# Performance work log

Measured on AMD Instinct MI355X. Metric: run time of the kernel, lower is better.

The kernel has to match this reference:

```python
import jax, jax.numpy as jnp
import numpy as np

EPS = 1e-5   # BatchNorm eps (eval mode, running_mean=0, running_var=1 as at init)
NEG = 0.2    # LeakyReLU negative slope


def _conv(W, x):
    # 1x1 conv == channel matmul. W: [out_c, in_c], x: [B, in_c, ...]
    return jnp.einsum('oc,bc...->bo...', W, x)


def _bn(x, g, b):
    # eval-mode BN with running_mean=0, running_var=1
    sh = (1, -1) + (1,) * (x.ndim - 2)
    return x * (g.reshape(sh) / np.float32(np.sqrt(1.0 + EPS))) + b.reshape(sh)


def _lrelu(x):
    return jax.nn.leaky_relu(x, NEG)


def _knn_idx(pos, k):
    # pos: [B, 3, N] -> idx [B, N, k] of k nearest points (incl. self)
    sq = jnp.sum(pos * pos, axis=1)                      # [B, N]
    inner = jnp.einsum('bcn,bcm->bnm', pos, pos)         # [B, N, N]
    dist = sq[:, :, None] + sq[:, None, :] - 2.0 * inner
    _, idx = jax.lax.top_k(-dist, k)
    return idx


def _gather(points, idx):
    # points [B, N, C], idx [B, N, K] -> [B, N, K, C]
    return jax.vmap(lambda p, i: p[i])(points, idx)


def setup_inputs() -> dict:
    key = jax.random.key(0)
    B, N, K = 2, 8192, 16
    d_points, d_model = 64, 64
    ks = jax.random.split(key, 24)
    w = lambda k_, o, i: (jax.random.normal(k_, (o, i), jnp.float32) * 0.05)
    gm = lambda k_, c: (1.0 + 0.1 * jax.random.normal(k_, (c,), jnp.float32))
    bt = lambda k_, c: (0.1 * jax.random.normal(k_, (c,), jnp.float32))
    return {
        'feats': jax.random.normal(ks[0], (B, d_points, N), jnp.float32),
        'pos': jax.random.uniform(ks[1], (B, 3, N), jnp.float32),
        'k': K,
        'W1': w(ks[2], d_model, d_points), 'g1': gm(ks[3], d_model), 'b1': bt(ks[4], d_model),
        'Wq': w(ks[5], d_model, d_model), 'Wk': w(ks[6], d_model, d_model), 'Wv': w(ks[7], d_model, d_model),
        'Wd1': w(ks[8], d_model, 3), 'gd1': gm(ks[9], d_model), 'bd1': bt(ks[10], d_model),
        'Wd2': w(ks[11], d_model, d_model), 'gd2': gm(ks[12], d_model), 'bd2': bt(ks[13], d_model),
        'Wg1': w(ks[14], d_model, d_model), 'gg1': gm(ks[15], d_model), 'bg1': bt(ks[16], d_model),
        'Wg2': w(ks[17], d_model, d_model), 'gg2': gm(ks[18], d_model), 'bg2': bt(ks[19], d_model),
        'W2': w(ks[20], d_points, d_model), 'g2': gm(ks[21], d_points), 'b2': bt(ks[22], d_points),
    }


def reference(feats, pos, k, W1, g1, b1, Wq, Wk, Wv,
              Wd1, gd1, bd1, Wd2, gd2, bd2,
              Wg1, gg1, bg1, Wg2, gg2, bg2, W2, g2, b2):
    B, _, N = feats.shape
    knn_idx = _knn_idx(pos, k)                            # [B, N, K]
    pos_nc = jnp.transpose(pos, (0, 2, 1))                # [B, N, 3]
    knn_pos = _gather(pos_nc, knn_idx)                    # [B, N, K, 3]

    x = _lrelu(_bn(_conv(W1, feats), g1, b1))             # [B, d, N]
    q = _conv(Wq, x)                                      # [B, d, N]
    k_feat = _gather(jnp.transpose(_conv(Wk, x), (0, 2, 1)), knn_idx)
    k_t = jnp.transpose(k_feat, (0, 3, 2, 1))             # [B, d, K, N]
    v_feat = _gather(jnp.transpose(_conv(Wv, x), (0, 2, 1)), knn_idx)
    v_t = jnp.transpose(v_feat, (0, 3, 2, 1))             # [B, d, K, N]

    rel = pos_nc[:, :, None, :] - knn_pos                 # [B, N, K, 3]
    rel_t = jnp.transpose(rel, (0, 3, 2, 1))              # [B, 3, K, N]
    pe = _lrelu(_bn(_conv(Wd1, rel_t), gd1, bd1))
    pos_enc = _lrelu(_bn(_conv(Wd2, pe), gd2, bd2))       # [B, d, K, N]

    a = q[:, :, None, :] - k_t + pos_enc                  # [B, d, K, N]
    a = _lrelu(_bn(_conv(Wg1, a), gg1, bg1))
    a = _lrelu(_bn(_conv(Wg2, a), gg2, bg2))
    # torch: attn / sqrt(k.size(-1)) where k has shape [B, d, K, N] -> sqrt(N)
    attn = jax.nn.softmax(a / jnp.sqrt(jnp.float32(N)), axis=-2)

    res = jnp.einsum('bmnf,bmnf->bmf', attn, v_t + pos_enc)  # [B, d, N]
    out = _lrelu(_bn(_conv(W2, res), g2, b2)) + feats
    return out
```

## Files before the change

kernel.cpp:

```cpp
#include <hip/hip_runtime.h>
#include <hip/hip_bf16.h>
#include <math.h>

namespace {

constexpr int B = 2;
constexpr int N = 8192;
constexpr int D = 64;
constexpr int GRID = 10;
constexpr int GC = GRID * GRID * GRID;
constexpr float H = 0.1f;
constexpr float NEGS = 0.2f;
constexpr float BN_INV = 0.9999950000374997f;
constexpr float RSQN = 0.011048543456039806f;

typedef __attribute__((ext_vector_type(8))) short bf16x8;
typedef __attribute__((ext_vector_type(16))) float f32x16;

union Frag { int4 i4; unsigned u[4]; bf16x8 h; };

__device__ __forceinline__ float lrelu(float v) { return fmaxf(v, NEGS * v); }

__device__ __forceinline__ unsigned pk2(float a, float b) {
  __hip_bfloat162 h2 = __float22bfloat162_rn(make_float2(a, b));
  unsigned r;
  __builtin_memcpy(&r, &h2, 4);
  return r;
}
__device__ __forceinline__ float blo(unsigned u) { return __uint_as_float(u << 16); }
__device__ __forceinline__ float bhi(unsigned u) { return __uint_as_float(u & 0xFFFF0000u); }

__device__ __forceinline__ f32x16 MF(int4 a, const Frag& b, f32x16 c) {
  Frag af; af.i4 = a;
  return __builtin_amdgcn_mfma_f32_32x32x16_bf16(af.h, b.h, c, 0, 0, 0);
}

template <int CTRL>
__device__ __forceinline__ float dpp_add(float v) {
  int t = __builtin_amdgcn_update_dpp(0, __float_as_int(v), CTRL, 0xF, 0xF, false);
  return v + __int_as_float(t);
}
__device__ __forceinline__ float rsum16(float v) {
  v = dpp_add<0x128>(v);
  v = dpp_add<0x124>(v);
  v = dpp_add<0x122>(v);
  v = dpp_add<0x121>(v);
  return v;
}
template <int CTRL>
__device__ __forceinline__ unsigned long long dpp_min_u64(unsigned long long k) {
  int lo = __builtin_amdgcn_update_dpp(0, (int)(unsigned)k, CTRL, 0xF, 0xF, false);
  int hi = __builtin_amdgcn_update_dpp(0, (int)(unsigned)(k >> 32), CTRL, 0xF, 0xF, false);
  unsigned long long o = ((unsigned long long)(unsigned)hi << 32) | (unsigned)lo;
  return o < k ? o : k;
}
__device__ __forceinline__ unsigned long long rmin16_u64(unsigned long long k) {
  k = dpp_min_u64<0x128>(k);
  k = dpp_min_u64<0x124>(k);
  k = dpp_min_u64<0x122>(k);
  k = dpp_min_u64<0x121>(k);
  return k;
}

__device__ __forceinline__ int cellco(float v) {
  int c = (int)(v * 10.0f);
  return min(max(c, 0), GRID - 1);
}

__device__ __forceinline__ void buildB(const f32x16& x0, const f32x16& x1, int h, Frag Bf[4]) {
  unsigned Z[8][2];
  #pragma unroll
  for (int q = 0; q < 4; ++q) {
    Z[q][0]     = pk2(x0[4*q+0], x0[4*q+1]);
    Z[q][1]     = pk2(x0[4*q+2], x0[4*q+3]);
    Z[4+q][0]   = pk2(x1[4*q+0], x1[4*q+1]);
    Z[4+q][1]   = pk2(x1[4*q+2], x1[4*q+3]);
  }
  unsigned S[8][2];
  #pragma unroll
  for (int q = 0; q < 8; ++q) {
    S[q][0] = (unsigned)__shfl_xor((int)Z[q][0], 32);
    S[q][1] = (unsigned)__shfl_xor((int)Z[q][1], 32);
  }
  #pragma unroll
  for (int t = 0; t < 4; ++t) {
    int qq = (t >> 1) * 4 + 2 * (t & 1);
    Bf[t].u[0] = h ? S[qq+1][0] : Z[qq][0];
    Bf[t].u[1] = h ? S[qq+1][1] : Z[qq][1];
    Bf[t].u[2] = h ? Z[qq+1][0] : S[qq][0];
    Bf[t].u[3] = h ? Z[qq+1][1] : S[qq][1];
  }
}

__device__ __forceinline__ f32x16 biasAct(f32x16 d, const float4* bp, int mt, int h) {
  f32x16 r;
  #pragma unroll
  for (int q = 0; q < 4; ++q) {
    float4 bb = bp[h * 8 + mt * 4 + q];
    r[4*q+0] = lrelu(d[4*q+0] + bb.x);
    r[4*q+1] = lrelu(d[4*q+1] + bb.y);
    r[4*q+2] = lrelu(d[4*q+2] + bb.z);
    r[4*q+3] = lrelu(d[4*q+3] + bb.w);
  }
  return r;
}

struct PrepArgs {
  const float* W[9];
  const float* scale[9];
  const float* bias[5];
  const float* bd1;
};

__global__ __launch_bounds__(256) void prep_kernel(PrepArgs a, unsigned short* AF, float* biasAll) {
  int mi = blockIdx.x;
  int tid = threadIdx.x;
  if (mi < 8) {
    int off = (mi == 7) ? 29696 : mi * 4096;
    const float* W = a.W[mi];
    const float* G = a.scale[mi];
    unsigned short* dst = AF + off;
    for (int e = tid; e < 4096; e += 256) {
      int i = e & 7, lane = (e >> 3) & 63, t = (e >> 9) & 3, mt = e >> 11;
      int row = 32 * mt + (lane & 31);
      int k = 16 * t + 8 * (lane >> 5) + i;
      float v = W[row * 64 + k];
      if (G) v *= G[row] * BN_INV;
      if (mi == 6) v *= RSQN;
      __hip_bfloat16 hb = __float2bfloat16(v);
      __builtin_memcpy(&dst[e], &hb, 2);
    }
  } else {
    const float* W = a.W[8];
    const float* G = a.scale[8];
    for (int e = tid; e < 1024; e += 256) {
      int i = e & 7, lane = (e >> 3) & 63, mt = e >> 9;
      int row = 32 * mt + (lane & 31), h = lane >> 5;
      float v = 0.f;
      if (h == 0) {
        if (i < 3) v = W[row * 3 + i] * G[row] * BN_INV;
        else if (i == 3) v = a.bd1[row];
      }
      __hip_bfloat16 hb = __float2bfloat16(v);
      __builtin_memcpy(&AF[28672 + e], &hb, 2);
    }
    for (int e = tid; e < 320; e += 256) {
      int ai = e >> 6, idx = e & 63;
      int h = idx >> 5, mt = (idx >> 4) & 1, q = (idx >> 2) & 3, j = idx & 3;
      float bv = a.bias[ai][32 * mt + 8 * q + 4 * h + j];
      if (ai == 3) bv *= RSQN;
      biasAll[e] = bv;
    }
  }
}

__global__ __launch_bounds__(256) void pos4cid_kernel(
    const float* __restrict__ pos, float* __restrict__ pos4,
    int* __restrict__ cid16, int* __restrict__ cellCount)
{
  int i = blockIdx.x * 256 + threadIdx.x;
  int b = i >> 13;
  int n = i & (N - 1);
  const float* pb = pos + (size_t)b * 3 * N;
  float x = pb[n], y = pb[N + n], z = pb[2 * N + n];
  float4 v = {x, y, z, x * x + y * y + z * z};
  *reinterpret_cast<float4*>(pos4 + (size_t)i * 4) = v;
  int cid = (cellco(z) * GRID + cellco(y)) * GRID + cellco(x);
  cid16[i] = cid;
  atomicAdd(&cellCount[b * GC + cid], 1);
}

__global__ __launch_bounds__(1024) void scan_kernel(
    const int* __restrict__ cnt, int* __restrict__ cellStart)
{
  __shared__ int s[2][2048];
  int t = threadIdx.x;
  s[0][t] = cnt[t];
  s[0][t + 1024] = cnt[t + 1024];
  __syncthreads();
  int src = 0;
  for (int off = 1; off < 2048; off <<= 1) {
    int dst = src ^ 1;
    for (int i = t; i < 2048; i += 1024) {
      int v = s[src][i];
      if (i >= off) v += s[src][i - off];
      s[dst][i] = v;
    }
    __syncthreads();
    src ^= 1;
  }
  cellStart[t] = (t == 0) ? 0 : s[src][t - 1];
  cellStart[t + 1024] = s[src][t + 1023];
}

__global__ __launch_bounds__(256) void scatter_kernel(
    const float* __restrict__ pos4, const int* __restrict__ cid16,
    const int* __restrict__ cellStart, int* __restrict__ cellOfs,
    float4* __restrict__ pos4s, int* __restrict__ sid, int* __restrict__ inv)
{
  int i = blockIdx.x * 256 + threadIdx.x;
  int b = i >> 13;
  int cg = b * GC + cid16[i];
  int dst = cellStart[cg] + atomicAdd(&cellOfs[cg], 1);
  pos4s[dst] = *reinterpret_cast<const float4*>(pos4 + (size_t)i * 4);
  sid[dst] = i & (N - 1);
  inv[i] = dst;
}

__global__ __launch_bounds__(256) void knn_shell_kernel(
    const float4* __restrict__ pos4s, const int* __restrict__ sid,
    const int* __restrict__ cellStart, int* __restrict__ knn_s)
{
  constexpr unsigned long long SENT = ~0ULL;
  int lq = threadIdx.x & 15;
  int wid = (blockIdx.x * 256 + threadIdx.x) >> 4;
  int b = wid >> 13;
  float4 q = pos4s[wid];
  int cx = cellco(q.x), cy = cellco(q.y), cz = cellco(q.z);
  const int cbase = b * GC;
  int* orow = knn_s + (size_t)wid * 16;

  bool done = false;
  #pragma unroll 1
  for (int r = 1; r < GRID; ++r) {
    if (!done) {
      unsigned long long dk[16];
      #pragma unroll
      for (int j = 0; j < 16; ++j) dk[j] = SENT;

      int x0 = max(cx - r, 0), x1 = min(cx + r, GRID - 1);
      int y0 = max(cy - r, 0), y1 = min(cy + r, GRID - 1);
      int z0 = max(cz - r, 0), z1 = min(cz + r, GRID - 1);
      #pragma unroll 1
      for (int zz = z0; zz <= z1; ++zz) {
        #pragma unroll 1
        for (int yy = y0; yy <= y1; ++yy) {
          int rowc = cbase + (zz * GRID + yy) * GRID;
          int i0 = cellStart[rowc + x0], i1 = cellStart[rowc + x1 + 1];
          #pragma unroll 1
          for (int i = i0 + lq; i < i1; i += 16) {
            float4 cp = pos4s[i];
            float inn = q.x * cp.x + q.y * cp.y + q.z * cp.z;
            float dist = fmaxf(fmaf(-2.f, inn, q.w + cp.w), 0.f);
            unsigned long long key =
                ((unsigned long long)__float_as_uint(dist) << 26) |
                ((unsigned long long)(unsigned)sid[i] << 13) |
                (unsigned long long)(unsigned)(i & (N - 1));
            if (key < dk[15]) {
              bool bj = true;
              #pragma unroll
              for (int j = 15; j >= 1; --j) {
                bool bjm1 = key < dk[j - 1];
                dk[j] = bj ? (bjm1 ? dk[j - 1] : key) : dk[j];
                bj = bjm1;
              }
              if (bj) dk[0] = key;
            }
          }
        }
      }

      float dlast = 0.f;
      #pragma unroll 1
      for (int e = 0; e < 16; ++e) {
        unsigned long long m = rmin16_u64(dk[0]);
        if (dk[0] == m) {
          #pragma unroll
          for (int j = 0; j < 15; ++j) dk[j] = dk[j + 1];
          dk[15] = SENT;
        }
        if (lq == 0) orow[e] = (int)(m & 0x1FFFULL);
        dlast = __uint_as_float((unsigned)(m >> 26));
      }

      float mg = 3.4e38f;
      if (cx - r > 0)        mg = fminf(mg, q.x - (cx - r) * H);
      if (cx + r < GRID - 1) mg = fminf(mg, (cx + r + 1) * H - q.x);
      if (cy - r > 0)        mg = fminf(mg, q.y - (cy - r) * H);
      if (cy + r < GRID - 1) mg = fminf(mg, (cy + r + 1) * H - q.y);
      if (cz - r > 0)        mg = fminf(mg, q.z - (cz - r) * H);
      if (cz + r < GRID - 1) mg = fminf(mg, (cz + r + 1) * H - q.z);
      done = (dlast <= mg * mg * 0.999f);
    }
    if (__all(done)) break;
  }
}

__global__ __launch_bounds__(256) void qkv_kernel(
    const float* __restrict__ feats, const int4* __restrict__ AF,
    const float* __restrict__ b1p, const int* __restrict__ inv,
    uint2* __restrict__ qT, uint2* __restrict__ kT, uint2* __restrict__ vT)
{
  __shared__ int4 sA[1024];
  int my = blockIdx.y;
  for (int i = threadIdx.x; i < 512; i += 256) {
    sA[i] = AF[i];
    sA[512 + i] = AF[512 * (1 + my) + i];
  }
  __syncthreads();
  int lane = threadIdx.x & 63, w = threadIdx.x >> 6;
  int gw = blockIdx.x * 4 + w;
  int col = lane & 31, h = lane >> 5;
  int nb = gw * 32;
  int b = nb >> 13;
  int n = (nb & (N - 1)) + col;
  size_t gpt = (size_t)b * N + n;
  int sv = inv[gpt];
  const float* fb = feats + (size_t)b * D * N + n;

  Frag Bf[4];
  #pragma unroll
  for (int t = 0; t < 4; ++t) {
    int c0 = 16 * t + 8 * h;
    float f[8];
    #pragma unroll
    for (int i = 0; i < 8; ++i) f[i] = fb[(size_t)(c0 + i) * N];
    #pragma unroll
    for (int d_ = 0; d_ < 4; ++d_) Bf[t].u[d_] = pk2(f[2*d_], f[2*d_+1]);
  }
  f32x16 acc0 = {}, acc1 = {};
  #pragma unroll
  for (int t = 0; t < 4; ++t) {
    acc0 = MF(sA[t * 64 + lane], Bf[t], acc0);
    acc1 = MF(sA[(4 + t) * 64 + lane], Bf[t], acc1);
  }
  const float4* bp = (const float4*)b1p;
  f32x16 x0 = biasAct(acc0, bp, 0, h);
  f32x16 x1 = biasAct(acc1, bp, 1, h);
  Frag Bx[4];
  buildB(x0, x1, h, Bx);

  uint2* op = (my == 0) ? qT : (my == 1) ? kT : vT;
  f32x16 a0 = {}, a1 = {};
  #pragma unroll
  for (int t = 0; t < 4; ++t) {
    a0 = MF(sA[512 + t * 64 + lane], Bx[t], a0);
    a1 = MF(sA[512 + (4 + t) * 64 + lane], Bx[t], a1);
  }
  #pragma unroll
  for (int q = 0; q < 4; ++q) {
    uint2 v0, v1;
    v0.x = pk2(a0[4*q+0], a0[4*q+1]); v0.y = pk2(a0[4*q+2], a0[4*q+3]);
    v1.x = pk2(a1[4*q+0], a1[4*q+1]); v1.y = pk2(a1[4*q+2], a1[4*q+3]);
    op[(size_t)sv * 16 + 2 * q + h] = v0;
    op[(size_t)sv * 16 + 8 + 2 * q + h] = v1;
  }
}

__global__ __launch_bounds__(256) void fused_kernel(
    const float4* __restrict__ pos4s, const int* __restrict__ sid,
    const int* __restrict__ knn_s,
    const uint2* __restrict__ qT, const uint2* __restrict__ kT, const uint2* __restrict__ vT,
    const int4* __restrict__ AF,
    const float* __restrict__ biases,
    uint2* __restrict__ res_ws)
{
  int lane = threadIdx.x & 63, w = threadIdx.x >> 6;
  int gw = blockIdx.x * 4 + w;
  int col = lane & 31, h = lane >> 5;
  int p = col >> 4, kk = col & 15;
  int sbase = gw * 2;
  int b = sbase >> 13;
  int s = sbase + p;

  int m_loc = knn_s[(size_t)s * 16 + kk];
  int orig = sid[s];
  float4 P = pos4s[s];

  __shared__ int4 sA[1664];
  for (int i = threadIdx.x; i < 1664; i += 256) sA[i] = AF[i];
  __syncthreads();
  const float4* bpd2 = (const float4*)(biases);
  const float4* bpg1 = (const float4*)(biases + 64);
  const float4* bpg2 = (const float4*)(biases + 128);

  size_t ms = (size_t)b * N + m_loc;
  float4 Q = pos4s[ms];
  float rx = P.x - Q.x, ry = P.y - Q.y, rz = P.z - Q.z;

  Frag B0;
  B0.u[0] = h ? 0u : pk2(rx, ry);
  B0.u[1] = h ? 0u : pk2(rz, 1.0f);
  B0.u[2] = 0u; B0.u[3] = 0u;
  f32x16 acc0 = {}, acc1 = {};
  acc0 = MF(sA[1536 + lane], B0, acc0);
  acc1 = MF(sA[1600 + lane], B0, acc1);
  f32x16 pe0, pe1;
  #pragma unroll
  for (int i = 0; i < 16; ++i) { pe0[i] = lrelu(acc0[i]); pe1[i] = lrelu(acc1[i]); }
  Frag Bp[4];
  buildB(pe0, pe1, h, Bp);

  acc0 = (f32x16){}; acc1 = (f32x16){};
  #pragma unroll
  for (int t = 0; t < 4; ++t) {
    acc0 = MF(sA[t * 64 + lane], Bp[t], acc0);
    acc1 = MF(sA[(4 + t) * 64 + lane], Bp[t], acc1);
  }
  f32x16 pn0 = biasAct(acc0, bpd2, 0, h);
  f32x16 pn1 = biasAct(acc1, bpd2, 1, h);

  unsigned pep[8][2];
  #pragma unroll
  for (int q = 0; q < 4; ++q) {
    pep[q][0]   = pk2(pn0[4*q+0], pn0[4*q+1]);
    pep[q][1]   = pk2(pn0[4*q+2], pn0[4*q+3]);
    pep[4+q][0] = pk2(pn1[4*q+0], pn1[4*q+1]);
    pep[4+q][1] = pk2(pn1[4*q+2], pn1[4*q+3]);
  }

  f32x16 av0, av1;
  #pragma unroll
  for (int mt = 0; mt < 2; ++mt) {
    f32x16& dst = mt ? av1 : av0;
    const f32x16& pn = mt ? pn1 : pn0;
    #pragma unroll
    for (int q = 0; q < 4; ++q) {
      uint2 qq_ = qT[(size_t)s * 16 + 8 * mt + 2 * q + h];
      uint2 kq_ = kT[ms * 16 + 8 * mt + 2 * q + h];
      dst[4*q+0] = pn[4*q+0] + blo(qq_.x) - blo(kq_.x);
      dst[4*q+1] = pn[4*q+1] + bhi(qq_.x) - bhi(kq_.x);
      dst[4*q+2] = pn[4*q+2] + blo(qq_.y) - blo(kq_.y);
      dst[4*q+3] = pn[4*q+3] + bhi(qq_.y) - bhi(kq_.y);
    }
  }
  buildB(av0, av1, h, Bp);

  acc0 = (f32x16){}; acc1 = (f32x16){};
  #pragma unroll
  for (int t = 0; t < 4; ++t) {
    acc0 = MF(sA[512 + t * 64 + lane], Bp[t], acc0);
    acc1 = MF(sA[512 + (4 + t) * 64 + lane], Bp[t], acc1);
  }
  f32x16 a10 = biasAct(acc0, bpg1, 0, h);
  f32x16 a11 = biasAct(acc1, bpg1, 1, h);
  buildB(a10, a11, h, Bp);

  acc0 = (f32x16){}; acc1 = (f32x16){};
  #pragma unroll
  for (int t = 0; t < 4; ++t) {
    acc0 = MF(sA[1024 + t * 64 + lane], Bp[t], acc0);
    acc1 = MF(sA[1024 + (4 + t) * 64 + lane], Bp[t], acc1);
  }
  f32x16 at0 = biasAct(acc0, bpg2, 0, h);
  f32x16 at1 = biasAct(acc1, bpg2, 1, h);

  uint2* rp = res_ws + ((size_t)b * N + orig) * 16;
  #pragma unroll
  for (int mt = 0; mt < 2; ++mt) {
    const f32x16& at = mt ? at1 : at0;
    f32x16 ev, nm;
    #pragma unroll
    for (int q = 0; q < 4; ++q) {
      uint2 vq_ = vT[ms * 16 + 8 * mt + 2 * q + h];
      unsigned pp0 = pep[mt * 4 + q][0], pp1 = pep[mt * 4 + q][1];
      float vp0 = blo(vq_.x) + blo(pp0);
      float vp1 = bhi(vq_.x) + bhi(pp0);
      float vp2 = blo(vq_.y) + blo(pp1);
      float vp3 = bhi(vq_.y) + bhi(pp1);
      ev[4*q+0] = __expf(at[4*q+0]); nm[4*q+0] = ev[4*q+0] * vp0;
      ev[4*q+1] = __expf(at[4*q+1]); nm[4*q+1] = ev[4*q+1] * vp1;
      ev[4*q+2] = __expf(at[4*q+2]); nm[4*q+2] = ev[4*q+2] * vp2;
      ev[4*q+3] = __expf(at[4*q+3]); nm[4*q+3] = ev[4*q+3] * vp3;
    }
    #pragma unroll
    for (int i = 0; i < 16; ++i) {
      ev[i] = rsum16(ev[i]);
      nm[i] = rsum16(nm[i]);
    }
    if (kk == 0) {
      #pragma unroll
      for (int q = 0; q < 4; ++q) {
        uint2 rr;
        rr.x = pk2(nm[4*q+0] / ev[4*q+0], nm[4*q+1] / ev[4*q+1]);
        rr.y = pk2(nm[4*q+2] / ev[4*q+2], nm[4*q+3] / ev[4*q+3]);
        rp[8 * mt + 2 * q + h] = rr;
      }
    }
  }
}

__global__ __launch_bounds__(256) void final_kernel(
    const uint2* __restrict__ res_ws, const int4* __restrict__ AF,
    const float* __restrict__ b2p, const float* __restrict__ feats,
    float* __restrict__ out)
{
  __shared__ int4 sA[512];
  for (int i = threadIdx.x; i < 512; i += 256) sA[i] = AF[i];
  __syncthreads();
  int lane = threadIdx.x & 63, w = threadIdx.x >> 6;
  int gw = blockIdx.x * 4 + w;
  int col = lane & 31, h = lane >> 5;
  int nb = gw * 32;
  int b = nb >> 13;
  int n = (nb & (N - 1)) + col;
  size_t g = (size_t)b * N + n;
  const int4* rp = (const int4*)(res_ws + (size_t)g * 16);
  Frag Br[4];
  #pragma unroll
  for (int t = 0; t < 4; ++t) Br[t].i4 = rp[2 * t + h];
  f32x16 a0 = {}, a1 = {};
  #pragma unroll
  for (int t = 0; t < 4; ++t) {
    a0 = MF(sA[t * 64 + lane], Br[t], a0);
    a1 = MF(sA[(4 + t) * 64 + lane], Br[t], a1);
  }
  const float4* bp = (const float4*)b2p;
  f32x16 o0 = biasAct(a0, bp, 0, h);
  f32x16 o1 = biasAct(a1, bp, 1, h);
  const float* fb = feats + (size_t)b * D * N;
  float* ob = out + (size_t)b * D * N;
  #pragma unroll
  for (int mt = 0; mt < 2; ++mt) {
    const f32x16& oo = mt ? o1 : o0;
    #pragma unroll
    for (int q = 0; q < 4; ++q) {
      #pragma unroll
      for (int j = 0; j < 4; ++j) {
        int chan = 32 * mt + 8 * q + 4 * h + j;
        ob[(size_t)chan * N + n] = oo[4*q+j] + fb[(size_t)chan * N + n];
      }
    }
  }
}

}

extern "C" void kernel_launch(void* const* d_in, const int* in_sizes, int n_in,
                              void* d_out, int out_size, void* d_ws, size_t ws_size,
                              hipStream_t stream) {
  const float* feats = (const float*)d_in[0];
  const float* pos   = (const float*)d_in[1];
  const float* W1  = (const float*)d_in[3];
  const float* g1  = (const float*)d_in[4];
  const float* b1  = (const float*)d_in[5];
  const float* Wq  = (const float*)d_in[6];
  const float* Wk  = (const float*)d_in[7];
  const float* Wv  = (const float*)d_in[8];
  const float* Wd1 = (const float*)d_in[9];
  const float* gd1 = (const float*)d_in[10];
  const float* bd1 = (const float*)d_in[11];
  const float* Wd2 = (const float*)d_in[12];
  const float* gd2 = (const float*)d_in[13];
  const float* bd2 = (const float*)d_in[14];
  const float* Wg1 = (const float*)d_in[15];
  const float* gg1 = (const float*)d_in[16];
  const float* bg1 = (const float*)d_in[17];
  const float* Wg2 = (const float*)d_in[18];
  const float* gg2 = (const float*)d_in[19];
  const float* bg2 = (const float*)d_in[20];
  const float* W2  = (const float*)d_in[21];
  const float* g2  = (const float*)d_in[22];
  const float* b2  = (const float*)d_in[23];

  uint8_t* wsb = (uint8_t*)d_ws;
  unsigned short* AF = (unsigned short*)wsb;
  float* biasAll = (float*)(wsb + 73728);
  float* pos4    = (float*)(wsb + 75008);
  uint2* qTb     = (uint2*)(wsb + 337152);
  uint2* kTb     = (uint2*)(wsb + 2434304);
  uint2* vTb     = (uint2*)(wsb + 4531456);
  uint2* res_ws  = (uint2*)(wsb + 6628608);
  int*   cid16     = (int*)(wsb + 10822912);
  int*   cellCount = (int*)(wsb + 10888448);
  int*   cellStart = (int*)(wsb + 10896640);
  int*   cellOfs   = (int*)(wsb + 10904832);
  float4* pos4s    = (float4*)(wsb + 10913024);
  int*   sid       = (int*)(wsb + 11175168);
  int*   knn_s     = (int*)(wsb + 11240704);
  int*   inv       = (int*)(wsb + 12289280);

  PrepArgs pa;
  pa.W[0] = W1;  pa.W[1] = Wq;  pa.W[2] = Wk;  pa.W[3] = Wv;
  pa.W[4] = Wd2; pa.W[5] = Wg1; pa.W[6] = Wg2; pa.W[7] = W2; pa.W[8] = Wd1;
  pa.scale[0] = g1;  pa.scale[1] = nullptr; pa.scale[2] = nullptr; pa.scale[3] = nullptr;
  pa.scale[4] = gd2; pa.scale[5] = gg1;     pa.scale[6] = gg2;     pa.scale[7] = g2; pa.scale[8] = gd1;
  pa.bias[0] = b1; pa.bias[1] = bd2; pa.bias[2] = bg1; pa.bias[3] = bg2; pa.bias[4] = b2;
  pa.bd1 = bd1;

  hipMemsetAsync(cellCount, 0, 2048 * sizeof(int), stream);
  hipMemsetAsync(cellOfs, 0, 2048 * sizeof(int), stream);
  hipLaunchKernelGGL(prep_kernel, dim3(9), dim3(256), 0, stream, pa, AF, biasAll);
  hipLaunchKernelGGL(pos4cid_kernel, dim3(B * N / 256), dim3(256), 0, stream,
                     pos, pos4, cid16, cellCount);
  hipLaunchKernelGGL(scan_kernel, dim3(1), dim3(1024), 0, stream, cellCount, cellStart);
  hipLaunchKernelGGL(scatter_kernel, dim3(B * N / 256), dim3(256), 0, stream,
                     pos4, cid16, cellStart, cellOfs, pos4s, sid, inv);
  hipLaunchKernelGGL(knn_shell_kernel, dim3(B * N / 16), dim3(256), 0, stream,
                     pos4s, sid, cellStart, knn_s);
  hipLaunchKernelGGL(qkv_kernel, dim3(128, 3), dim3(256), 0, stream,
                     feats, (const int4*)wsb, biasAll, inv, qTb, kTb, vTb);
  hipLaunchKernelGGL(fused_kernel, dim3(B * N / 8), dim3(256), 0, stream,
                     pos4s, sid, knn_s, qTb, kTb, vTb,
                     (const int4*)(wsb + 32768), biasAll + 64, res_ws);
  hipLaunchKernelGGL(final_kernel, dim3(128), dim3(256), 0, stream,
                     res_ws, (const int4*)(wsb + 59392), biasAll + 256, feats, (float*)d_out);
}
```

Measured before the change: 147.6 us.

## Merge kNN and QKV kernels into one launch, skip small shells at boundaries

The kNN shell search and the QKV projection now run as one grid: the first blocks do kNN and the last 384 blocks do the QKV matmuls, so the two independent stages can overlap and one launch is saved. Queries whose cell lies on two or more grid borders start the search at radius 2 instead of 1, which skips a shell pass that is likely to fail the termination test. The kNN output write changes from 16 scalar stores by one lane to one coalesced store per lane. The merged kernel carries the QKV kernel's shared-memory footprint and register pressure into the kNN blocks, which may lower occupancy for the kNN part.

```diff
diff --git a/kernel.cpp b/kernel.cpp
--- a/kernel.cpp
+++ b/kernel.cpp
@@ -13,6 +13,7 @@
 constexpr float NEGS = 0.2f;
 constexpr float BN_INV = 0.9999950000374997f;
 constexpr float RSQN = 0.011048543456039806f;
+constexpr int KNN_BLOCKS = B * N / 16;
 
 typedef __attribute__((ext_vector_type(8))) short bf16x8;
 typedef __attribute__((ext_vector_type(16))) float f32x16;
@@ -207,103 +208,112 @@
   inv[i] = dst;
 }
 
-__global__ __launch_bounds__(256) void knn_shell_kernel(
+__global__ __launch_bounds__(256) void knnqkv_kernel(
     const float4* __restrict__ pos4s, const int* __restrict__ sid,
-    const int* __restrict__ cellStart, int* __restrict__ knn_s)
-{
-  constexpr unsigned long long SENT = ~0ULL;
-  int lq = threadIdx.x & 15;
-  int wid = (blockIdx.x * 256 + threadIdx.x) >> 4;
-  int b = wid >> 13;
-  float4 q = pos4s[wid];
-  int cx = cellco(q.x), cy = cellco(q.y), cz = cellco(q.z);
-  const int cbase = b * GC;
-  int* orow = knn_s + (size_t)wid * 16;
-
-  bool done = false;
-  #pragma unroll 1
-  for (int r = 1; r < GRID; ++r) {
-    if (!done) {
-      unsigned long long dk[16];
-      #pragma unroll
-      for (int j = 0; j < 16; ++j) dk[j] = SENT;
-
-      int x0 = max(cx - r, 0), x1 = min(cx + r, GRID - 1);
-      int y0 = max(cy - r, 0), y1 = min(cy + r, GRID - 1);
-      int z0 = max(cz - r, 0), z1 = min(cz + r, GRID - 1);
-      #pragma unroll 1
-      for (int zz = z0; zz <= z1; ++zz) {
-        #pragma unroll 1
-        for (int yy = y0; yy <= y1; ++yy) {
-          int rowc = cbase + (zz * GRID + yy) * GRID;
-          int i0 = cellStart[rowc + x0], i1 = cellStart[rowc + x1 + 1];
-          #pragma unroll 1
-          for (int i = i0 + lq; i < i1; i += 16) {
-            float4 cp = pos4s[i];
-            float inn = q.x * cp.x + q.y * cp.y + q.z * cp.z;
-            float dist = fmaxf(fmaf(-2.f, inn, q.w + cp.w), 0.f);
-            unsigned long long key =
-                ((unsigned long long)__float_as_uint(dist) << 26) |
-                ((unsigned long long)(unsigned)sid[i] << 13) |
-                (unsigned long long)(unsigned)(i & (N - 1));
-            if (key < dk[15]) {
-              bool bj = true;
-              #pragma unroll
-              for (int j = 15; j >= 1; --j) {
-                bool bjm1 = key < dk[j - 1];
-                dk[j] = bj ? (bjm1 ? dk[j - 1] : key) : dk[j];
-                bj = bjm1;
-              }
-              if (bj) dk[0] = key;
-            }
-          }
-        }
-      }
-
-      float dlast = 0.f;
-      #pragma unroll 1
-      for (int e = 0; e < 16; ++e) {
-        unsigned long long m = rmin16_u64(dk[0]);
-        if (dk[0] == m) {
-          #pragma unroll
-          for (int j = 0; j < 15; ++j) dk[j] = dk[j + 1];
-          dk[15] = SENT;
-        }
-        if (lq == 0) orow[e] = (int)(m & 0x1FFFULL);
-        dlast = __uint_as_float((unsigned)(m >> 26));
-      }
-
-      float mg = 3.4e38f;
-      if (cx - r > 0)        mg = fminf(mg, q.x - (cx - r) * H);
-      if (cx + r < GRID - 1) mg = fminf(mg, (cx + r + 1) * H - q.x);
-      if (cy - r > 0)        mg = fminf(mg, q.y - (cy - r) * H);
-      if (cy + r < GRID - 1) mg = fminf(mg, (cy + r + 1) * H - q.y);
-      if (cz - r > 0)        mg = fminf(mg, q.z - (cz - r) * H);
-      if (cz + r < GRID - 1) mg = fminf(mg, (cz + r + 1) * H - q.z);
-      done = (dlast <= mg * mg * 0.999f);
-    }
-    if (__all(done)) break;
-  }
-}
-
-__global__ __launch_bounds__(256) void qkv_kernel(
+    const int* __restrict__ cellStart, int* __restrict__ knn_s,
     const float* __restrict__ feats, const int4* __restrict__ AF,
     const float* __restrict__ b1p, const int* __restrict__ inv,
     uint2* __restrict__ qT, uint2* __restrict__ kT, uint2* __restrict__ vT)
 {
   __shared__ int4 sA[1024];
-  int my = blockIdx.y;
+
+  if (blockIdx.x < KNN_BLOCKS) {
+    constexpr unsigned long long SENT = ~0ULL;
+    int lq = threadIdx.x & 15;
+    int wid = (blockIdx.x * 256 + threadIdx.x) >> 4;
+    int b = wid >> 13;
+    float4 q = pos4s[wid];
+    int cx = cellco(q.x), cy = cellco(q.y), cz = cellco(q.z);
+    const int cbase = b * GC;
+    int myout = 0;
+
+    int nb = (int)(cx == 0 || cx == GRID - 1) + (int)(cy == 0 || cy == GRID - 1)
+           + (int)(cz == 0 || cz == GRID - 1);
+    int r0 = (nb >= 2) ? 2 : 1;
+
+    bool done = false;
+    #pragma unroll 1
+    for (int r = r0; r < GRID; ++r) {
+      if (!done) {
+        unsigned long long dk[16];
+        #pragma unroll
+        for (int j = 0; j < 16; ++j) dk[j] = SENT;
+
+        int x0 = max(cx - r, 0), x1 = min(cx + r, GRID - 1);
+        int y0 = max(cy - r, 0), y1 = min(cy + r, GRID - 1);
+        int z0 = max(cz - r, 0), z1 = min(cz + r, GRID - 1);
+        #pragma unroll 1
+        for (int zz = z0; zz <= z1; ++zz) {
+          #pragma unroll 1
+          for (int yy = y0; yy <= y1; ++yy) {
+            int rowc = cbase + (zz * GRID + yy) * GRID;
+            int i0 = cellStart[rowc + x0], i1 = cellStart[rowc + x1 + 1];
+            #pragma unroll 1
+            for (int i = i0 + lq; i < i1; i += 16) {
+              float4 cp = pos4s[i];
+              float inn = q.x * cp.x + q.y * cp.y + q.z * cp.z;
+              float dist = fmaxf(fmaf(-2.f, inn, q.w + cp.w), 0.f);
+              unsigned long long key =
+                  ((unsigned long long)__float_as_uint(dist) << 26) |
+                  ((unsigned long long)(unsigned)sid[i] << 13) |
+                  (unsigned long long)(unsigned)(i & (N - 1));
+              if (key < dk[15]) {
+                bool bj = true;
+                #pragma unroll
+                for (int j = 15; j >= 1; --j) {
+                  bool bjm1 = key < dk[j - 1];
+                  dk[j] = bj ? (bjm1 ? dk[j - 1] : key) : dk[j];
+                  bj = bjm1;
+                }
+                if (bj) dk[0] = key;
+              }
+            }
+          }
+        }
+
+        float dlast = 0.f;
+        #pragma unroll 1
+        for (int e = 0; e < 16; ++e) {
+          unsigned long long m = rmin16_u64(dk[0]);
+          if (dk[0] == m) {
+            #pragma unroll
+            for (int j = 0; j < 15; ++j) dk[j] = dk[j + 1];
+            dk[15] = SENT;
+          }
+          if (lq == e) myout = (int)(m & 0x1FFFULL);
+          dlast = __uint_as_float((unsigned)(m >> 26));
+        }
+
+        float mg = 3.4e38f;
+        if (cx - r > 0)        mg = fminf(mg, q.x - (cx - r) * H);
+        if (cx + r < GRID - 1) mg = fminf(mg, (cx + r + 1) * H - q.x);
+        if (cy - r > 0)        mg = fminf(mg, q.y - (cy - r) * H);
+        if (cy + r < GRID - 1) mg = fminf(mg, (cy + r + 1) * H - q.y);
+        if (cz - r > 0)        mg = fminf(mg, q.z - (cz - r) * H);
+        if (cz + r < GRID - 1) mg = fminf(mg, (cz + r + 1) * H - q.z);
+        done = (dlast <= mg * mg * 0.999f);
+      }
+      if (__all(done)) break;
+    }
+
+    knn_s[(size_t)wid * 16 + lq] = myout;
+    return;
+  }
+
+  int qb = blockIdx.x - KNN_BLOCKS;
+  int my = qb >> 7;
+  int gx = qb & 127;
   for (int i = threadIdx.x; i < 512; i += 256) {
     sA[i] = AF[i];
     sA[512 + i] = AF[512 * (1 + my) + i];
   }
   __syncthreads();
   int lane = threadIdx.x & 63, w = threadIdx.x >> 6;
-  int gw = blockIdx.x * 4 + w;
+  int gw = gx * 4 + w;
   int col = lane & 31, h = lane >> 5;
-  int nb = gw * 32;
-  int b = nb >> 13;
-  int n = (nb & (N - 1)) + col;
+  int nb_ = gw * 32;
+  int b = nb_ >> 13;
+  int n = (nb_ & (N - 1)) + col;
   size_t gpt = (size_t)b * N + n;
   int sv = inv[gpt];
   const float* fb = feats + (size_t)b * D * N + n;
@@ -586,9 +596,8 @@
   hipLaunchKernelGGL(scan_kernel, dim3(1), dim3(1024), 0, stream, cellCount, cellStart);
   hipLaunchKernelGGL(scatter_kernel, dim3(B * N / 256), dim3(256), 0, stream,
                      pos4, cid16, cellStart, cellOfs, pos4s, sid, inv);
-  hipLaunchKernelGGL(knn_shell_kernel, dim3(B * N / 16), dim3(256), 0, stream,
-                     pos4s, sid, cellStart, knn_s);
-  hipLaunchKernelGGL(qkv_kernel, dim3(128, 3), dim3(256), 0, stream,
+  hipLaunchKernelGGL(knnqkv_kernel, dim3(KNN_BLOCKS + 384), dim3(256), 0, stream,
+                     pos4s, sid, cellStart, knn_s,
                      feats, (const int4*)wsb, biasAll, inv, qTb, kTb, vTb);
   hipLaunchKernelGGL(fused_kernel, dim3(B * N / 8), dim3(256), 0, stream,
                      pos4s, sid, knn_s, qTb, kTb, vTb,
```

Measured after the change: 144.6 us. -2.1%, faster.
